# Kernel tuning notes

Hardware: AMD Instinct MI355X
Metric: run time of the kernel (lower is better)

The kernel has to match this reference:

```python
import jax, jax.numpy as jnp
import numpy as np

N = 16384      # batch size
F = 1024       # n_features
H = 256        # n_dim (latent)


def setup_inputs() -> dict:
    key = jax.random.key(0)
    ks = jax.random.split(key, 6)
    X = jax.random.normal(ks[0], (N, F), dtype=jnp.float32)
    We = jax.random.normal(ks[1], (F, H), dtype=jnp.float32) / np.sqrt(F).astype(np.float32)
    be = jnp.zeros((H,), dtype=jnp.float32)
    Wd = jax.random.normal(ks[2], (H, F), dtype=jnp.float32) / np.sqrt(H).astype(np.float32)
    bd = jnp.zeros((F,), dtype=jnp.float32)
    Wc = jax.random.normal(ks[3], (H, 1), dtype=jnp.float32) / np.sqrt(H).astype(np.float32)
    bc = jnp.zeros((1,), dtype=jnp.float32)
    s = jax.random.randint(ks[4], (N,), 0, 2, dtype=jnp.int32)  # protected attribute labels in {0,1}
    return {"X": X, "We": We, "be": be, "Wd": Wd, "bd": bd, "Wc": Wc, "bc": bc, "s": s, "p": 1}


def reference(X, We, be, Wd, bd, Wc, bc, s, p):
    # encoder / decoder (single Linear each, as in the default NRL construction)
    g = X @ We + be                      # [N, H]
    rec = g @ Wd + bd                    # [N, F]
    mse_mean = jnp.mean((rec - X) ** 2)  # MSELoss is built with reduction='sum' but forward uses torch.mean(pow(...)) directly

    # critic scores for ALL rows (critics share weights: [module]*n_protected)
    c = (g @ Wc + bc)[:, 0]              # [N]

    # masked pairwise L1: sum_{i in P, j notin P} |c_i - c_j|
    mp = (s == p)                        # rows where s == p
    mpf = mp.astype(c.dtype)
    mrf = (~mp).astype(c.dtype)
    Dmat = jnp.abs(c[:, None] - c[None, :])   # [N, N] pairwise L1 (cdist equivalent)
    total = mpf @ (Dmat @ mrf)                # mp^T D mr == cdist(c_p, c_rest, p=1).sum()

    w_dist_count = mp.sum()                   # == w_dist.shape[0] (number of protected rows)
    w_dist_mean = total / w_dist_count.astype(c.dtype)

    return (mse_mean, jnp.asarray(rec.shape[0]), w_dist_mean, w_dist_count)
```

## Files before the change

### kernel.cpp

```cpp
#include <hip/hip_runtime.h>
#include <hip/hip_bf16.h>
#include <cstdint>

#define NR 16384
#define NF 1024
#define NH 256

typedef __bf16 bf16x8 __attribute__((ext_vector_type(8)));
typedef float f32x4 __attribute__((ext_vector_type(4)));
typedef unsigned short us8 __attribute__((ext_vector_type(8)));

static __device__ __forceinline__ unsigned short f2bf(float f) {
    unsigned u = __float_as_uint(f);
    u += 0x7FFFu + ((u >> 16) & 1u);
    return (unsigned short)(u >> 16);
}


__global__ __launch_bounds__(256) void prep_kernel(
    const float* __restrict__ We, const float* __restrict__ Wd,
    unsigned short* __restrict__ Wepk, unsigned short* __restrict__ Wdpk,
    float* __restrict__ hdr) {
    const int b = blockIdx.x, t = threadIdx.x;
    if (b == 0 && t < 192) hdr[t] = 0.f;
    if (b < 128) {
        const int k0 = b, c = t;
        const int kc = k0 >> 2, q = k0 & 3, nb = c >> 4, li = c & 15;
        us8 v;
#pragma unroll
        for (int e = 0; e < 8; e++)
            v[e] = f2bf(We[(size_t)(k0 * 8 + e) * NH + c]);
        *(us8*)&Wepk[((size_t)(nb * 32 + kc)) * 512 + (q * 16 + li) * 8] = v;
    } else {
        const int idx = b - 128;
        const int k0 = idx >> 2, c = (idx & 3) * 256 + t;
        const int kc = k0 >> 2, q = k0 & 3, nb = c >> 4, li = c & 15;
        us8 v;
#pragma unroll
        for (int e = 0; e < 8; e++)
            v[e] = f2bf(Wd[(size_t)(k0 * 8 + e) * NF + c]);
        *(us8*)&Wdpk[((size_t)(nb * 8 + kc)) * 512 + (q * 16 + li) * 8] = v;
    }
}

__global__ __launch_bounds__(512, 2) void fused_kernel(
    const float* __restrict__ X,
    const unsigned short* __restrict__ Wepk, const unsigned short* __restrict__ Wdpk,
    const float* __restrict__ be, const float* __restrict__ bd,
    const float* __restrict__ Wc, const int* __restrict__ s, const int* __restrict__ pv,
    float* __restrict__ cP, float* __restrict__ cR, float* __restrict__ hdr) {
    __shared__ union {
        unsigned short xa[16384];
        struct {
            unsigned short gs[16384];
            float credu[8][64];
            float msred[8];
        } p2;
    } u;
    const int t = threadIdx.x;
    const int b = blockIdx.x, m0 = b * 64;
    const int w = t >> 6, lane = t & 63, q = lane >> 4, li = lane & 15;

    const int srow = w * 8;
    const int kcgl = lane >> 3;
    const int sq2  = (lane >> 1) & 3;
    const int sh   = lane & 1;

    {
        const float* xq = X + (size_t)m0 * NF + lane * 4;
#pragma unroll
        for (int rr = 0; rr < 8; ++rr) {
            const int r = srow + rr;
            float4 v4 = *(const float4*)(xq + (size_t)r * NF);
            ushort4 st = { f2bf(v4.x), f2bf(v4.y), f2bf(v4.z), f2bf(v4.w) };
            const int p = (sq2 * 16 + (r & 15)) ^ kcgl;
            *(ushort4*)&u.xa[(kcgl * 4 + (r >> 4)) * 512 + p * 8 + sh * 4] = st;
        }
    }
    __syncthreads();

    const unsigned short* Bp[2];
#pragma unroll
    for (int j = 0; j < 2; j++)
        Bp[j] = Wepk + ((size_t)(w * 2 + j) * 32) * 512 + lane * 8;

    us8 fb[8][2];
#pragma unroll
    for (int z = 0; z < 8; ++z)
#pragma unroll
        for (int j = 0; j < 2; j++) fb[z][j] = *(const us8*)(Bp[j] + z * 512);

    f32x4 acc[4][2] = {};
    float4 xn[8];

#pragma unroll
    for (int ks = 0; ks < 4; ++ks) {
        if (ks < 3) {
#pragma unroll
            for (int rr = 0; rr < 8; ++rr)
                xn[rr] = *(const float4*)(X + (size_t)(m0 + srow + rr) * NF +
                                          (ks + 1) * 256 + lane * 4);
        }
#pragma unroll
        for (int kcl = 0; kcl < 8; ++kcl) {
            const int kcg = ks * 8 + kcl;
            const int cb = kcg & 7;
            bf16x8 a[4];
#pragma unroll
            for (int mi = 0; mi < 4; ++mi)
                a[mi] = __builtin_bit_cast(bf16x8,
                    *(const us8*)&u.xa[(kcl * 4 + mi) * 512 + (lane ^ kcl) * 8]);
#pragma unroll
            for (int j = 0; j < 2; ++j) {
                bf16x8 bf = __builtin_bit_cast(bf16x8, fb[cb][j]);
#pragma unroll
                for (int mi = 0; mi < 4; ++mi)
                    acc[mi][j] = __builtin_amdgcn_mfma_f32_16x16x32_bf16(bf, a[mi], acc[mi][j], 0, 0, 0);
            }
            if (kcg + 8 < 32) {
#pragma unroll
                for (int j = 0; j < 2; j++) fb[cb][j] = *(const us8*)(Bp[j] + (kcg + 8) * 512);
            }
        }
        __syncthreads();
        if (ks < 3) {
#pragma unroll
            for (int rr = 0; rr < 8; ++rr) {
                const int r = srow + rr;
                ushort4 st = { f2bf(xn[rr].x), f2bf(xn[rr].y),
                               f2bf(xn[rr].z), f2bf(xn[rr].w) };
                const int p = (sq2 * 16 + (r & 15)) ^ kcgl;
                *(ushort4*)&u.xa[(kcgl * 4 + (r >> 4)) * 512 + p * 8 + sh * 4] = st;
            }
            __syncthreads();
        }
    }

#pragma unroll
    for (int mi = 0; mi < 4; ++mi) {
        float csum = 0.f;
#pragma unroll
        for (int j = 0; j < 2; ++j) {
            const int colb = w * 32 + j * 16 + q * 4;
            float4 be4 = *(const float4*)&be[colb];
            float4 wc4 = *(const float4*)&Wc[colb];
            float v0 = acc[mi][j][0] + be4.x;
            float v1 = acc[mi][j][1] + be4.y;
            float v2 = acc[mi][j][2] + be4.z;
            float v3 = acc[mi][j][3] + be4.w;
            csum += v0 * wc4.x + v1 * wc4.y + v2 * wc4.z + v3 * wc4.w;
            ushort4 st = { f2bf(v0), f2bf(v1), f2bf(v2), f2bf(v3) };
            const int q2e = j * 2 + (q >> 1);
            const int p = (q2e * 16 + li) ^ w;
            *(ushort4*)&u.p2.gs[(w * 4 + mi) * 512 + p * 8 + (q & 1) * 4] = st;
        }
        csum += __shfl_down(csum, 32);
        csum += __shfl_down(csum, 16);
        if (lane < 16) u.p2.credu[w][mi * 16 + lane] = csum;
    }
    __syncthreads();

    if (t < 64) {
        float cs = 0.f;
#pragma unroll
        for (int ww = 0; ww < 8; ++ww) cs += u.p2.credu[ww][t];
        bool pr = (s[m0 + t] == pv[0]);
        unsigned long long mk = __ballot(pr);
        int np = __popcll(mk);
        int baseP = 0, baseR = 0;
        if (t == 0) {
            baseP = atomicAdd((int*)hdr + 129, np);
            baseR = atomicAdd((int*)hdr + 130, 64 - np);
        }
        baseP = __shfl(baseP, 0);
        baseR = __shfl(baseR, 0);
        int offP = __popcll(mk & ((1ull << t) - 1ull));
        int offR = t - offP;
        if (pr) cP[baseP + offP] = cs; else cR[baseR + offR] = cs;
    }

    float lsum = 0.f;
    const unsigned short* Wp = Wdpk + lane * 8;
#pragma unroll
    for (int pass = 0; pass < 2; ++pass) {
        const int nb0 = pass * 32 + w * 4;
        us8 gb[4][4];
#pragma unroll
        for (int z = 0; z < 4; ++z)
#pragma unroll
            for (int j = 0; j < 4; ++j)
                gb[z][j] = *(const us8*)(Wp + ((size_t)((nb0 + j) * 8 + z)) * 512);
        f32x4 a2[4][4] = {};
#pragma unroll
        for (int kc = 0; kc < 8; ++kc) {
            const int cb = kc & 3;
            bf16x8 af[4];
#pragma unroll
            for (int mi = 0; mi < 4; ++mi)
                af[mi] = __builtin_bit_cast(bf16x8,
                    *(const us8*)&u.p2.gs[(kc * 4 + mi) * 512 + (lane ^ kc) * 8]);
#pragma unroll
            for (int j = 0; j < 4; ++j) {
                bf16x8 bf = __builtin_bit_cast(bf16x8, gb[cb][j]);
#pragma unroll
                for (int mi = 0; mi < 4; ++mi)
                    a2[mi][j] = __builtin_amdgcn_mfma_f32_16x16x32_bf16(bf, af[mi], a2[mi][j], 0, 0, 0);
            }
            if (kc + 4 < 8) {
#pragma unroll
                for (int j = 0; j < 4; ++j)
                    gb[cb][j] = *(const us8*)(Wp + ((size_t)((nb0 + j) * 8 + kc + 4)) * 512);
            }
        }
#pragma unroll
        for (int mi = 0; mi < 4; ++mi) {
            const size_t rowoff = (size_t)(m0 + mi * 16 + li) * NF;
#pragma unroll
            for (int j = 0; j < 4; ++j) {
                const int colb = pass * 512 + w * 64 + j * 16 + q * 4;
                float4 bd4 = *(const float4*)&bd[colb];
                float4 xr  = *(const float4*)&X[rowoff + colb];
                float d0 = a2[mi][j][0] + bd4.x - xr.x;
                float d1 = a2[mi][j][1] + bd4.y - xr.y;
                float d2 = a2[mi][j][2] + bd4.z - xr.z;
                float d3 = a2[mi][j][3] + bd4.w - xr.w;
                lsum += d0 * d0 + d1 * d1 + d2 * d2 + d3 * d3;
            }
        }
    }
#pragma unroll
    for (int o = 32; o; o >>= 1) lsum += __shfl_down(lsum, o);
    if (lane == 0) u.p2.msred[w] = lsum;
    __syncthreads();
    if (t == 0) {
        float ms = 0.f;
#pragma unroll
        for (int ww = 0; ww < 8; ++ww) ms += u.p2.msred[ww];
        atomicAdd(&hdr[b & 63], ms);
    }
}

__global__ __launch_bounds__(256) void pair_fin_kernel(
    const float* __restrict__ cP, const float* __restrict__ cR,
    float* __restrict__ hdr, float* __restrict__ out) {
    __shared__ float sj[1024];
    __shared__ float red[256];
    __shared__ int win;
    const int nP = ((const int*)hdr)[129];
    const int nR = ((const int*)hdr)[130];
    const int jb = blockIdx.x * 1024;
    int jn = nR - jb; if (jn < 0) jn = 0; if (jn > 1024) jn = 1024;
    float sum = 0.f;
    if (jn > 0 && blockIdx.y * 512 < nP) {
        for (int j = threadIdx.x; j < 1024; j += 256)
            sj[j] = (jb + j < nR) ? cR[jb + j] : 0.f;
        __syncthreads();
        const int a0 = blockIdx.y * 512 + threadIdx.x, a1 = a0 + 256;
        const float ca0 = (a0 < nP) ? cP[a0] : 0.f;
        const float ca1 = (a1 < nP) ? cP[a1] : 0.f;
        float s0 = 0.f, s1 = 0.f;
#pragma unroll 8
        for (int j4 = 0; j4 < 256; j4++) {
            float4 v = *(const float4*)&sj[j4 * 4];
            s0 += fabsf(ca0 - v.x) + fabsf(ca0 - v.y) + fabsf(ca0 - v.z) + fabsf(ca0 - v.w);
            s1 += fabsf(ca1 - v.x) + fabsf(ca1 - v.y) + fabsf(ca1 - v.z) + fabsf(ca1 - v.w);
        }
        float pad = (float)(1024 - jn);
        s0 -= pad * fabsf(ca0);
        s1 -= pad * fabsf(ca1);
        if (a0 >= nP) s0 = 0.f;
        if (a1 >= nP) s1 = 0.f;
        sum = s0 + s1;
#pragma unroll
        for (int o = 32; o; o >>= 1) sum += __shfl_down(sum, o);
        if ((threadIdx.x & 63) == 0 && sum != 0.f)
            atomicAdd(&hdr[64 + ((blockIdx.y * 16 + blockIdx.x) & 63)], sum);
    }
    __threadfence();
    __syncthreads();
    if (threadIdx.x == 0)
        win = (atomicAdd((int*)(hdr + 128), 1) == 16 * 32 - 1) ? 1 : 0;
    __syncthreads();
    if (win) {
        float v = (threadIdx.x < 128) ? atomicAdd(&hdr[threadIdx.x], 0.f) : 0.f;
        red[threadIdx.x] = v;
        __syncthreads();
        if (threadIdx.x == 0) {
            float ms = 0.f, ps = 0.f;
            for (int i = 0; i < 64; i++) { ms += red[i]; ps += red[64 + i]; }
            int np = atomicAdd((int*)(hdr + 129), 0);
            out[0] = ms / (float)((size_t)NR * NF);
            out[1] = (float)NR;
            out[2] = ps / (float)np;
            out[3] = (float)np;
        }
    }
}

extern "C" void kernel_launch(void* const* d_in, const int* in_sizes, int n_in,
                              void* d_out, int out_size, void* d_ws, size_t ws_size,
                              hipStream_t stream) {
    const float* X  = (const float*)d_in[0];
    const float* We = (const float*)d_in[1];
    const float* be = (const float*)d_in[2];
    const float* Wd = (const float*)d_in[3];
    const float* bd = (const float*)d_in[4];
    const float* Wc = (const float*)d_in[5];
    const int*   s  = (const int*)d_in[7];
    const int*   pv = (const int*)d_in[8];

    char* ws = (char*)d_ws;
    float* hdr = (float*)ws;
    float* cP  = (float*)(ws + 1024);
    float* cR  = (float*)(ws + 1024 + 65536);
    unsigned short* Wepk = (unsigned short*)(ws + 1024 + 2 * 65536);
    unsigned short* Wdpk = Wepk + (size_t)NH * NF;

    prep_kernel<<<256, 256, 0, stream>>>(We, Wd, Wepk, Wdpk, hdr);
    fused_kernel<<<256, 512, 0, stream>>>(X, Wepk, Wdpk, be, bd, Wc, s, pv, cP, cR, hdr);
    pair_fin_kernel<<<dim3(16, 32), 256, 0, stream>>>(cP, cR, hdr, (float*)d_out);
}
```

Measured before the change: 183.5 us.

## Shrink register footprint by halving weight prefetch depth and decoder tile width

Cuts the encoder's weight-fragment prefetch ring from 8 to 4 stages, narrows each decoder pass from 4 to 2 column tiles (4 passes instead of 2), interleaves LDS A-fragment loads with their MFMAs, and scopes the X prefetch buffer per iteration. The min-blocks hint in launch_bounds is dropped. The goal is lower VGPR pressure, avoiding spills or allowing better scheduling. The cost is less latency hiding for the global weight loads and more decoder passes, each reloading the LDS A fragments.

```diff
diff --git a/kernel.cpp b/kernel.cpp
--- a/kernel.cpp
+++ b/kernel.cpp
@@ -43,7 +43,7 @@
     }
 }
 
-__global__ __launch_bounds__(512, 2) void fused_kernel(
+__global__ __launch_bounds__(512) void fused_kernel(
     const float* __restrict__ X,
     const unsigned short* __restrict__ Wepk, const unsigned short* __restrict__ Wdpk,
     const float* __restrict__ be, const float* __restrict__ bd,
@@ -84,17 +84,17 @@
     for (int j = 0; j < 2; j++)
         Bp[j] = Wepk + ((size_t)(w * 2 + j) * 32) * 512 + lane * 8;
 
-    us8 fb[8][2];
-#pragma unroll
-    for (int z = 0; z < 8; ++z)
+    us8 fb[4][2];
+#pragma unroll
+    for (int z = 0; z < 4; ++z)
 #pragma unroll
         for (int j = 0; j < 2; j++) fb[z][j] = *(const us8*)(Bp[j] + z * 512);
 
     f32x4 acc[4][2] = {};
-    float4 xn[8];
 
 #pragma unroll
     for (int ks = 0; ks < 4; ++ks) {
+        float4 xn[8];
         if (ks < 3) {
 #pragma unroll
             for (int rr = 0; rr < 8; ++rr)
@@ -104,22 +104,19 @@
 #pragma unroll
         for (int kcl = 0; kcl < 8; ++kcl) {
             const int kcg = ks * 8 + kcl;
-            const int cb = kcg & 7;
-            bf16x8 a[4];
-#pragma unroll
-            for (int mi = 0; mi < 4; ++mi)
-                a[mi] = __builtin_bit_cast(bf16x8,
+            const int cb = kcg & 3;
+#pragma unroll
+            for (int mi = 0; mi < 4; ++mi) {
+                bf16x8 a = __builtin_bit_cast(bf16x8,
                     *(const us8*)&u.xa[(kcl * 4 + mi) * 512 + (lane ^ kcl) * 8]);
-#pragma unroll
-            for (int j = 0; j < 2; ++j) {
-                bf16x8 bf = __builtin_bit_cast(bf16x8, fb[cb][j]);
-#pragma unroll
-                for (int mi = 0; mi < 4; ++mi)
-                    acc[mi][j] = __builtin_amdgcn_mfma_f32_16x16x32_bf16(bf, a[mi], acc[mi][j], 0, 0, 0);
-            }
-            if (kcg + 8 < 32) {
-#pragma unroll
-                for (int j = 0; j < 2; j++) fb[cb][j] = *(const us8*)(Bp[j] + (kcg + 8) * 512);
+                acc[mi][0] = __builtin_amdgcn_mfma_f32_16x16x32_bf16(
+                    __builtin_bit_cast(bf16x8, fb[cb][0]), a, acc[mi][0], 0, 0, 0);
+                acc[mi][1] = __builtin_amdgcn_mfma_f32_16x16x32_bf16(
+                    __builtin_bit_cast(bf16x8, fb[cb][1]), a, acc[mi][1], 0, 0, 0);
+            }
+            if (kcg + 4 < 32) {
+#pragma unroll
+                for (int j = 0; j < 2; j++) fb[cb][j] = *(const us8*)(Bp[j] + (kcg + 4) * 512);
             }
         }
         __syncthreads();
@@ -182,33 +179,30 @@
     float lsum = 0.f;
     const unsigned short* Wp = Wdpk + lane * 8;
 #pragma unroll
-    for (int pass = 0; pass < 2; ++pass) {
-        const int nb0 = pass * 32 + w * 4;
-        us8 gb[4][4];
+    for (int pass = 0; pass < 4; ++pass) {
+        const int nb0 = pass * 16 + w * 2;
+        us8 gb[4][2];
 #pragma unroll
         for (int z = 0; z < 4; ++z)
 #pragma unroll
-            for (int j = 0; j < 4; ++j)
+            for (int j = 0; j < 2; ++j)
                 gb[z][j] = *(const us8*)(Wp + ((size_t)((nb0 + j) * 8 + z)) * 512);
-        f32x4 a2[4][4] = {};
+        f32x4 a2[4][2] = {};
 #pragma unroll
         for (int kc = 0; kc < 8; ++kc) {
             const int cb = kc & 3;
-            bf16x8 af[4];
-#pragma unroll
-            for (int mi = 0; mi < 4; ++mi)
-                af[mi] = __builtin_bit_cast(bf16x8,
+#pragma unroll
+            for (int mi = 0; mi < 4; ++mi) {
+                bf16x8 af = __builtin_bit_cast(bf16x8,
                     *(const us8*)&u.p2.gs[(kc * 4 + mi) * 512 + (lane ^ kc) * 8]);
-#pragma unroll
-            for (int j = 0; j < 4; ++j) {
-                bf16x8 bf = __builtin_bit_cast(bf16x8, gb[cb][j]);
-#pragma unroll
-                for (int mi = 0; mi < 4; ++mi)
-                    a2[mi][j] = __builtin_amdgcn_mfma_f32_16x16x32_bf16(bf, af[mi], a2[mi][j], 0, 0, 0);
+                a2[mi][0] = __builtin_amdgcn_mfma_f32_16x16x32_bf16(
+                    __builtin_bit_cast(bf16x8, gb[cb][0]), af, a2[mi][0], 0, 0, 0);
+                a2[mi][1] = __builtin_amdgcn_mfma_f32_16x16x32_bf16(
+                    __builtin_bit_cast(bf16x8, gb[cb][1]), af, a2[mi][1], 0, 0, 0);
             }
             if (kc + 4 < 8) {
 #pragma unroll
-                for (int j = 0; j < 4; ++j)
+                for (int j = 0; j < 2; ++j)
                     gb[cb][j] = *(const us8*)(Wp + ((size_t)((nb0 + j) * 8 + kc + 4)) * 512);
             }
         }
@@ -216,8 +210,8 @@
         for (int mi = 0; mi < 4; ++mi) {
             const size_t rowoff = (size_t)(m0 + mi * 16 + li) * NF;
 #pragma unroll
-            for (int j = 0; j < 4; ++j) {
-                const int colb = pass * 512 + w * 64 + j * 16 + q * 4;
+            for (int j = 0; j < 2; ++j) {
+                const int colb = pass * 256 + w * 32 + j * 16 + q * 4;
                 float4 bd4 = *(const float4*)&bd[colb];
                 float4 xr  = *(const float4*)&X[rowoff + colb];
                 float d0 = a2[mi][j][0] + bd4.x - xr.x;
```

Measured after the change: 177.6 us. 3.2% less time.
